# Performance work log

Hardware: AMD Instinct MI355X
Metric: run time of the kernel (lower is better)

## Reference

```python
import jax, jax.numpy as jnp
import numpy as np

LN_EPS = 1e-5

def _mlp(h, W1, b1, g1, beta1, W2, b2):
    # Linear -> LayerNorm -> SiLU -> Linear (make_mlp with 2 layers, output_activation=None)
    h = h @ W1 + b1
    mu = h.mean(-1, keepdims=True)
    var = h.var(-1, keepdims=True)  # biased var, matches torch LayerNorm
    h = (h - mu) * jax.lax.rsqrt(var + LN_EPS) * g1 + beta1
    h = jax.nn.silu(h)
    return h @ W2 + b2

def setup_inputs() -> dict:
    key = jax.random.key(0)
    ks = jax.random.split(key, 8)
    N, E, H = 50000, 800000, 128
    def init_w(k, fan_in, fan_out):
        lim = 1.0 / np.sqrt(fan_in)
        return jax.random.uniform(k, (fan_in, fan_out), jnp.float32, -lim, lim)
    return {
        "x": jax.random.normal(ks[0], (N, H), jnp.float32),
        "edge_index": jax.random.randint(ks[1], (2, E), 0, N),
        "e": jax.random.normal(ks[2], (E, H), jnp.float32),
        # node network: in 2H (cat of x and sum-aggregated messages)
        "Wn1": init_w(ks[3], 2 * H, H), "bn1": jnp.zeros((H,), jnp.float32),
        "gn1": jnp.ones((H,), jnp.float32), "betan1": jnp.zeros((H,), jnp.float32),
        "Wn2": init_w(ks[4], H, H), "bn2": jnp.zeros((H,), jnp.float32),
        # edge network: in 3H (cat of x_out[start], x_out[end], e)
        "We1": init_w(ks[5], 3 * H, H), "be1": jnp.zeros((H,), jnp.float32),
        "ge1": jnp.ones((H,), jnp.float32), "betae1": jnp.zeros((H,), jnp.float32),
        "We2": init_w(ks[6], H, H), "be2": jnp.zeros((H,), jnp.float32),
    }

def reference(x, edge_index, e, Wn1, bn1, gn1, betan1, Wn2, bn2, We1, be1, ge1, betae1, We2, be2):
    start, end = edge_index[0], edge_index[1]
    # aggregation == 'sum': scatter_add of edge features onto destination nodes
    msgs = jax.ops.segment_sum(e, end, num_segments=x.shape[0])  # [N, H]
    node_inputs = jnp.concatenate([x, msgs], axis=-1)  # [N, 2H]
    x_out = _mlp(node_inputs, Wn1, bn1, gn1, betan1, Wn2, bn2) + x  # residual
    edge_inputs = jnp.concatenate([x_out[start], x_out[end], e], axis=-1)  # [E, 3H]
    e_out = _mlp(edge_inputs, We1, be1, ge1, betae1, We2, be2) + e  # residual
    return (x_out, e_out)
```

## Files before the change

kernel.cpp:

```cpp
#include <hip/hip_runtime.h>

#define H 128
#define LN_EPS 1e-5f

typedef __attribute__((ext_vector_type(8))) short bf16x8;
typedef __attribute__((ext_vector_type(4))) float f32x4;

__device__ __forceinline__ ushort f2bf(float f) {
    unsigned u = __builtin_bit_cast(unsigned, f);
    u += 0x7fffu + ((u >> 16) & 1u);
    return (ushort)(u >> 16);
}

__device__ __forceinline__ float bf2f(ushort u) {
    return __builtin_bit_cast(float, (unsigned)u << 16);
}

__device__ __forceinline__ unsigned cvt_pk(float lo, float hi) {
    unsigned r;
    asm("v_cvt_pk_bf16_f32 %0, %1, %2" : "=v"(r) : "v"(lo), "v"(hi));
    return r;
}

__device__ __forceinline__ f32x4 mfma16(bf16x8 a, bf16x8 b, f32x4 c) {
    return __builtin_amdgcn_mfma_f32_16x16x32_bf16(a, b, c, 0, 0, 0);
}

__global__ __launch_bounds__(256) void hist_kernel(
    const int* __restrict__ ei, int* __restrict__ cnt, int E)
{
    int i = blockIdx.x * 256 + threadIdx.x;
    if (i < E) atomicAdd(&cnt[ei[E + i]], 1);
}

__global__ __launch_bounds__(1024) void scan_kernel(
    const int* __restrict__ cnt, int* __restrict__ off,
    int* __restrict__ cursor, int N)
{
    __shared__ int s[1024];
    const int t = threadIdx.x;
    const int chunk = (N + 1023) / 1024;
    const int lo = t * chunk, hi = min(lo + chunk, N);
    int sum = 0;
    for (int i = lo; i < hi; ++i) sum += cnt[i];
    s[t] = sum;
    __syncthreads();
    for (int d = 1; d < 1024; d <<= 1) {
        int v = (t >= d) ? s[t - d] : 0;
        __syncthreads();
        s[t] += v;
        __syncthreads();
    }
    int running = s[t] - sum;
    for (int i = lo; i < hi; ++i) {
        off[i] = running;
        cursor[i] = running;
        running += cnt[i];
    }
    if (t == 1023) off[N] = running;
}

__global__ __launch_bounds__(256) void reorder_kernel(
    const int* __restrict__ ei, int* __restrict__ cursor,
    int* __restrict__ sorted, int E)
{
    int i = blockIdx.x * 256 + threadIdx.x;
    if (i < E) {
        int pos = atomicAdd(&cursor[ei[E + i]], 1);
        sorted[pos] = i;
    }
}

__global__ __launch_bounds__(256) void segsum_kernel(
    const float* __restrict__ e, const int* __restrict__ sorted,
    const int* __restrict__ off, float* __restrict__ msgs, int N)
{
    int node = blockIdx.x * 4 + (threadIdx.x >> 6);
    int lane = threadIdx.x & 63;
    if (node >= N) return;
    int beg = off[node], end = off[node + 1];
    float ax = 0.f, ay = 0.f;
    for (int base = beg; base < end; base += 64) {
        int eid_l = (base + lane < end) ? sorted[base + lane] : 0;
        int cnt = min(64, end - base);
        int i = 0;
        for (; i + 4 <= cnt; i += 4) {
            int e0 = __shfl(eid_l, i), e1 = __shfl(eid_l, i + 1);
            int e2 = __shfl(eid_l, i + 2), e3 = __shfl(eid_l, i + 3);
            float2 v0 = *reinterpret_cast<const float2*>(e + (size_t)e0 * H + lane * 2);
            float2 v1 = *reinterpret_cast<const float2*>(e + (size_t)e1 * H + lane * 2);
            float2 v2 = *reinterpret_cast<const float2*>(e + (size_t)e2 * H + lane * 2);
            float2 v3 = *reinterpret_cast<const float2*>(e + (size_t)e3 * H + lane * 2);
            ax += v0.x + v1.x + v2.x + v3.x;
            ay += v0.y + v1.y + v2.y + v3.y;
        }
        for (; i < cnt; ++i) {
            int eid = __shfl(eid_l, i);
            float2 v = *reinterpret_cast<const float2*>(e + (size_t)eid * H + lane * 2);
            ax += v.x; ay += v.y;
        }
    }
    *reinterpret_cast<float2*>(msgs + (size_t)node * H + lane * 2) = make_float2(ax, ay);
}

__global__ __launch_bounds__(256) void wtrans_kernel(
    const float* __restrict__ W, ushort* __restrict__ Wt, int K)
{
    int idx = blockIdx.x * 256 + threadIdx.x;
    if (idx >= K * H) return;
    int k = idx >> 7, n = idx & (H - 1);
    Wt[n * K + k] = f2bf(W[idx]);
}

__global__ __launch_bounds__(256, 3) void node_mlp_kernel(
    const float* __restrict__ x, const float* __restrict__ msgs,
    const ushort* __restrict__ W1t, const float* __restrict__ b1,
    const float* __restrict__ g1, const float* __restrict__ be1,
    const ushort* __restrict__ W2t, const float* __restrict__ b2,
    const ushort* __restrict__ We1t,
    float* __restrict__ x_out,
    ushort* __restrict__ Pa, ushort* __restrict__ Pb, int N)
{
    __shared__ ushort smem[64 * 264];
    __shared__ float part_s[2][64], part_q[2][64];

    const int tid = threadIdx.x;
    const int row0 = blockIdx.x * 64;

    for (int idx = tid; idx < 64 * 64; idx += 256) {
        int r = idx >> 6, c4 = idx & 63;
        int row = row0 + r;
        float4 v = make_float4(0.f, 0.f, 0.f, 0.f);
        if (row < N)
            v = (c4 < 32) ? reinterpret_cast<const float4*>(x + (size_t)row * H)[c4]
                          : reinterpret_cast<const float4*>(msgs + (size_t)row * H)[c4 - 32];
        uint2 pk = make_uint2(cvt_pk(v.x, v.y), cvt_pk(v.z, v.w));
        *reinterpret_cast<uint2*>(&smem[r * 264 + c4 * 4]) = pk;
    }
    __syncthreads();

    const int lane = tid & 63, w = tid >> 6;
    const int l15 = lane & 15, lg = lane >> 4;
    const int mrow = (w & 1) * 32, ncol = (w >> 1) * 64;
    const int rA0 = mrow + l15, rA1 = mrow + 16 + l15;

    const ushort* pi0 = smem + (size_t)rA0 * 264;
    const ushort* pi1 = smem + (size_t)rA1 * 264;
    const ushort* pw1 = W1t + (size_t)(ncol + l15) * 256;

    f32x4 acc[2][4];
    #pragma unroll
    for (int mt = 0; mt < 2; ++mt)
        #pragma unroll
        for (int nt = 0; nt < 4; ++nt)
            acc[mt][nt] = (f32x4){0.f, 0.f, 0.f, 0.f};

    #pragma unroll
    for (int ks = 0; ks < 8; ++ks) {
        int k0 = ks * 32 + lg * 8;
        bf16x8 a0 = *reinterpret_cast<const bf16x8*>(pi0 + k0);
        bf16x8 a1 = *reinterpret_cast<const bf16x8*>(pi1 + k0);
        #pragma unroll
        for (int nt = 0; nt < 4; ++nt) {
            bf16x8 bfr = *reinterpret_cast<const bf16x8*>(pw1 + (size_t)nt * 16 * 256 + k0);
            acc[0][nt] = mfma16(a0, bfr, acc[0][nt]);
            acc[1][nt] = mfma16(a1, bfr, acc[1][nt]);
        }
    }

    float b1c[4], g1c[4], be1c[4];
    #pragma unroll
    for (int nt = 0; nt < 4; ++nt) {
        int c = ncol + nt * 16 + l15;
        b1c[nt] = b1[c]; g1c[nt] = g1[c]; be1c[nt] = be1[c];
    }
    #pragma unroll
    for (int mt = 0; mt < 2; ++mt)
        #pragma unroll
        for (int nt = 0; nt < 4; ++nt)
            #pragma unroll
            for (int r = 0; r < 4; ++r)
                acc[mt][nt][r] += b1c[nt];

    #pragma unroll
    for (int mt = 0; mt < 2; ++mt) {
        #pragma unroll
        for (int r = 0; r < 4; ++r) {
            float s = acc[mt][0][r] + acc[mt][1][r] + acc[mt][2][r] + acc[mt][3][r];
            float q = acc[mt][0][r] * acc[mt][0][r] + acc[mt][1][r] * acc[mt][1][r]
                    + acc[mt][2][r] * acc[mt][2][r] + acc[mt][3][r] * acc[mt][3][r];
            #pragma unroll
            for (int m = 8; m >= 1; m >>= 1) {
                s += __shfl_xor(s, m);
                q += __shfl_xor(q, m);
            }
            if (l15 == 0) {
                int rl = mrow + mt * 16 + lg * 4 + r;
                part_s[w >> 1][rl] = s;
                part_q[w >> 1][rl] = q;
            }
        }
    }
    __syncthreads();

    #pragma unroll
    for (int mt = 0; mt < 2; ++mt) {
        #pragma unroll
        for (int r = 0; r < 4; ++r) {
            int rl = mrow + mt * 16 + lg * 4 + r;
            float s  = part_s[0][rl] + part_s[1][rl];
            float q  = part_q[0][rl] + part_q[1][rl];
            float mu = s * (1.0f / H);
            float rs = rsqrtf(q * (1.0f / H) - mu * mu + LN_EPS);
            #pragma unroll
            for (int nt = 0; nt < 4; ++nt) {
                float v = (acc[mt][nt][r] - mu) * rs * g1c[nt] + be1c[nt];
                v = v / (1.0f + __expf(-v));
                smem[rl * 136 + ncol + nt * 16 + l15] = f2bf(v);
            }
        }
    }
    __syncthreads();

    const ushort* ph0 = smem + (size_t)rA0 * 136;
    const ushort* ph1 = smem + (size_t)rA1 * 136;
    const ushort* pw2 = W2t + (size_t)(ncol + l15) * 128;

    f32x4 acc2[2][4];
    #pragma unroll
    for (int nt = 0; nt < 4; ++nt) {
        float bb = b2[ncol + nt * 16 + l15];
        #pragma unroll
        for (int mt = 0; mt < 2; ++mt)
            acc2[mt][nt] = (f32x4){bb, bb, bb, bb};
    }
    #pragma unroll
    for (int ks = 0; ks < 4; ++ks) {
        int k0 = ks * 32 + lg * 8;
        bf16x8 a0 = *reinterpret_cast<const bf16x8*>(ph0 + k0);
        bf16x8 a1 = *reinterpret_cast<const bf16x8*>(ph1 + k0);
        #pragma unroll
        for (int nt = 0; nt < 4; ++nt) {
            bf16x8 bfr = *reinterpret_cast<const bf16x8*>(pw2 + (size_t)nt * 16 * 128 + k0);
            acc2[0][nt] = mfma16(a0, bfr, acc2[0][nt]);
            acc2[1][nt] = mfma16(a1, bfr, acc2[1][nt]);
        }
    }

    #pragma unroll
    for (int mt = 0; mt < 2; ++mt) {
        #pragma unroll
        for (int r = 0; r < 4; ++r) {
            int row = row0 + mrow + mt * 16 + lg * 4 + r;
            if (row < N) {
                const float* rp = x + (size_t)row * H;
                float* op = x_out + (size_t)row * H;
                #pragma unroll
                for (int nt = 0; nt < 4; ++nt) {
                    int c = ncol + nt * 16 + l15;
                    float o = acc2[mt][nt][r] + rp[c];
                    op[c] = o;
                    acc2[mt][nt][r] = o;
                }
            }
        }
    }
    __syncthreads();

    #pragma unroll
    for (int mt = 0; mt < 2; ++mt) {
        #pragma unroll
        for (int r = 0; r < 4; ++r) {
            int rl = mrow + mt * 16 + lg * 4 + r;
            #pragma unroll
            for (int nt = 0; nt < 4; ++nt)
                smem[rl * 136 + ncol + nt * 16 + l15] = f2bf(acc2[mt][nt][r]);
        }
    }
    __syncthreads();

    const ushort* px0 = smem + (size_t)rA0 * 136 + lg * 8;
    const ushort* px1 = smem + (size_t)rA1 * 136 + lg * 8;
    const ushort* pwa = We1t + (size_t)(ncol + l15) * 384 + lg * 8;
    const ushort* pwb = pwa + 128;

    f32x4 aa[2][4], ab[2][4];
    #pragma unroll
    for (int mt = 0; mt < 2; ++mt)
        #pragma unroll
        for (int nt = 0; nt < 4; ++nt) {
            aa[mt][nt] = (f32x4){0.f, 0.f, 0.f, 0.f};
            ab[mt][nt] = (f32x4){0.f, 0.f, 0.f, 0.f};
        }

    #pragma unroll
    for (int t = 0; t < 4; ++t) {
        bf16x8 a0 = *reinterpret_cast<const bf16x8*>(px0 + t * 32);
        bf16x8 a1 = *reinterpret_cast<const bf16x8*>(px1 + t * 32);
        #pragma unroll
        for (int nt = 0; nt < 4; ++nt) {
            bf16x8 ba = *reinterpret_cast<const bf16x8*>(pwa + (size_t)nt * 16 * 384 + t * 32);
            bf16x8 bb = *reinterpret_cast<const bf16x8*>(pwb + (size_t)nt * 16 * 384 + t * 32);
            aa[0][nt] = mfma16(a0, ba, aa[0][nt]);
            aa[1][nt] = mfma16(a1, ba, aa[1][nt]);
            ab[0][nt] = mfma16(a0, bb, ab[0][nt]);
            ab[1][nt] = mfma16(a1, bb, ab[1][nt]);
        }
    }

    #pragma unroll
    for (int mt = 0; mt < 2; ++mt) {
        #pragma unroll
        for (int r = 0; r < 4; ++r) {
            int row = row0 + mrow + mt * 16 + lg * 4 + r;
            if (row < N) {
                ushort* pa = Pa + (size_t)row * H;
                ushort* pb = Pb + (size_t)row * H;
                #pragma unroll
                for (int nt = 0; nt < 4; ++nt) {
                    int c = ncol + nt * 16 + l15;
                    pa[c] = f2bf(aa[mt][nt][r]);
                    pb[c] = f2bf(ab[mt][nt][r]);
                }
            }
        }
    }
}

__global__ __launch_bounds__(256, 4) void edge_mlp_kernel(
    const ushort* __restrict__ Pa, const ushort* __restrict__ Pb,
    const float* __restrict__ e, const int* __restrict__ ei,
    const ushort* __restrict__ W1t,
    const float* __restrict__ b1,
    const float* __restrict__ g1, const float* __restrict__ be1,
    const ushort* __restrict__ W2t, const float* __restrict__ b2,
    float* __restrict__ e_out, int E)
{
    __shared__ ushort es[64 * 136];
    __shared__ ushort ps[64 * 136];
    __shared__ float part_s[2][64], part_q[2][64];

    const int tid = threadIdx.x;
    const int row0 = blockIdx.x * 64;

    for (int idx = tid; idx < 64 * 16; idx += 256) {
        int r = idx >> 4, c = idx & 15;
        int rr = min(row0 + r, E - 1);
        int s = ei[rr], d = ei[E + rr];
        bf16x8 va = *reinterpret_cast<const bf16x8*>(Pa + (size_t)s * H + c * 8);
        bf16x8 vb = *reinterpret_cast<const bf16x8*>(Pb + (size_t)d * H + c * 8);
        float f0 = bf2f((ushort)va[0]) + bf2f((ushort)vb[0]);
        float f1 = bf2f((ushort)va[1]) + bf2f((ushort)vb[1]);
        float f2 = bf2f((ushort)va[2]) + bf2f((ushort)vb[2]);
        float f3 = bf2f((ushort)va[3]) + bf2f((ushort)vb[3]);
        float f4 = bf2f((ushort)va[4]) + bf2f((ushort)vb[4]);
        float f5 = bf2f((ushort)va[5]) + bf2f((ushort)vb[5]);
        float f6 = bf2f((ushort)va[6]) + bf2f((ushort)vb[6]);
        float f7 = bf2f((ushort)va[7]) + bf2f((ushort)vb[7]);
        uint4 pk = make_uint4(cvt_pk(f0, f1), cvt_pk(f2, f3),
                              cvt_pk(f4, f5), cvt_pk(f6, f7));
        *reinterpret_cast<uint4*>(&ps[r * 136 + c * 8]) = pk;
    }

    for (int idx = tid; idx < 64 * 32; idx += 256) {
        int r = idx >> 5, c4 = idx & 31;
        int row = row0 + r;
        float4 v = make_float4(0.f, 0.f, 0.f, 0.f);
        if (row < E)
            v = reinterpret_cast<const float4*>(e + (size_t)row * H)[c4];
        uint2 pk = make_uint2(cvt_pk(v.x, v.y), cvt_pk(v.z, v.w));
        *reinterpret_cast<uint2*>(&es[r * 136 + c4 * 4]) = pk;
    }
    __syncthreads();

    const int lane = tid & 63, w = tid >> 6;
    const int l15 = lane & 15, lg = lane >> 4;
    const int mrow = (w & 1) * 32, ncol = (w >> 1) * 64;
    const int rA0 = mrow + l15, rA1 = mrow + 16 + l15;

    const ushort* pe0 = es + (size_t)rA0 * 136 + lg * 8;
    const ushort* pe1 = es + (size_t)rA1 * 136 + lg * 8;
    const ushort* pw1 = W1t + (size_t)(ncol + l15) * 384 + 256 + lg * 8;

    f32x4 acc[2][4];
    #pragma unroll
    for (int mt = 0; mt < 2; ++mt)
        #pragma unroll
        for (int nt = 0; nt < 4; ++nt)
            acc[mt][nt] = (f32x4){0.f, 0.f, 0.f, 0.f};

    #pragma unroll
    for (int t = 0; t < 4; ++t) {
        bf16x8 a0 = *reinterpret_cast<const bf16x8*>(pe0 + t * 32);
        bf16x8 a1 = *reinterpret_cast<const bf16x8*>(pe1 + t * 32);
        #pragma unroll
        for (int nt = 0; nt < 4; ++nt) {
            bf16x8 bfr = *reinterpret_cast<const bf16x8*>(pw1 + (size_t)nt * 16 * 384 + t * 32);
            acc[0][nt] = mfma16(a0, bfr, acc[0][nt]);
            acc[1][nt] = mfma16(a1, bfr, acc[1][nt]);
        }
    }

    float b1c[4], g1c[4], be1c[4];
    #pragma unroll
    for (int nt = 0; nt < 4; ++nt) {
        int c = ncol + nt * 16 + l15;
        b1c[nt] = b1[c]; g1c[nt] = g1[c]; be1c[nt] = be1[c];
    }
    #pragma unroll
    for (int mt = 0; mt < 2; ++mt)
        #pragma unroll
        for (int r = 0; r < 4; ++r) {
            int rl = mrow + mt * 16 + lg * 4 + r;
            #pragma unroll
            for (int nt = 0; nt < 4; ++nt)
                acc[mt][nt][r] += b1c[nt] + bf2f(ps[rl * 136 + ncol + nt * 16 + l15]);
        }

    #pragma unroll
    for (int mt = 0; mt < 2; ++mt) {
        #pragma unroll
        for (int r = 0; r < 4; ++r) {
            float s = acc[mt][0][r] + acc[mt][1][r] + acc[mt][2][r] + acc[mt][3][r];
            float q = acc[mt][0][r] * acc[mt][0][r] + acc[mt][1][r] * acc[mt][1][r]
                    + acc[mt][2][r] * acc[mt][2][r] + acc[mt][3][r] * acc[mt][3][r];
            #pragma unroll
            for (int m = 8; m >= 1; m >>= 1) {
                s += __shfl_xor(s, m);
                q += __shfl_xor(q, m);
            }
            if (l15 == 0) {
                int rl = mrow + mt * 16 + lg * 4 + r;
                part_s[w >> 1][rl] = s;
                part_q[w >> 1][rl] = q;
            }
        }
    }
    __syncthreads();

    #pragma unroll
    for (int mt = 0; mt < 2; ++mt) {
        #pragma unroll
        for (int r = 0; r < 4; ++r) {
            int rl = mrow + mt * 16 + lg * 4 + r;
            float s  = part_s[0][rl] + part_s[1][rl];
            float q  = part_q[0][rl] + part_q[1][rl];
            float mu = s * (1.0f / H);
            float rs = rsqrtf(q * (1.0f / H) - mu * mu + LN_EPS);
            #pragma unroll
            for (int nt = 0; nt < 4; ++nt) {
                float v = (acc[mt][nt][r] - mu) * rs * g1c[nt] + be1c[nt];
                v = v / (1.0f + __expf(-v));
                es[rl * 136 + ncol + nt * 16 + l15] = f2bf(v);
            }
        }
    }
    __syncthreads();

    const ushort* ph0 = es + (size_t)rA0 * 136;
    const ushort* ph1 = es + (size_t)rA1 * 136;
    const ushort* pw2 = W2t + (size_t)(ncol + l15) * 128;

    f32x4 acc2[2][4];
    #pragma unroll
    for (int nt = 0; nt < 4; ++nt) {
        float bb = b2[ncol + nt * 16 + l15];
        #pragma unroll
        for (int mt = 0; mt < 2; ++mt)
            acc2[mt][nt] = (f32x4){bb, bb, bb, bb};
    }
    #pragma unroll
    for (int ks = 0; ks < 4; ++ks) {
        int k0 = ks * 32 + lg * 8;
        bf16x8 a0 = *reinterpret_cast<const bf16x8*>(ph0 + k0);
        bf16x8 a1 = *reinterpret_cast<const bf16x8*>(ph1 + k0);
        #pragma unroll
        for (int nt = 0; nt < 4; ++nt) {
            bf16x8 bfr = *reinterpret_cast<const bf16x8*>(pw2 + (size_t)nt * 16 * 128 + k0);
            acc2[0][nt] = mfma16(a0, bfr, acc2[0][nt]);
            acc2[1][nt] = mfma16(a1, bfr, acc2[1][nt]);
        }
    }

    #pragma unroll
    for (int mt = 0; mt < 2; ++mt) {
        #pragma unroll
        for (int r = 0; r < 4; ++r) {
            int row = row0 + mrow + mt * 16 + lg * 4 + r;
            if (row < E) {
                const float* rp = e + (size_t)row * H;
                float* op = e_out + (size_t)row * H;
                #pragma unroll
                for (int nt = 0; nt < 4; ++nt) {
                    int c = ncol + nt * 16 + l15;
                    op[c] = acc2[mt][nt][r] + rp[c];
                }
            }
        }
    }
}

extern "C" void kernel_launch(void* const* d_in, const int* in_sizes, int n_in,
                              void* d_out, int out_size, void* d_ws, size_t ws_size,
                              hipStream_t stream)
{
    const float* x     = (const float*)d_in[0];
    const int*   ei    = (const int*)  d_in[1];
    const float* e     = (const float*)d_in[2];
    const float* Wn1   = (const float*)d_in[3];
    const float* bn1   = (const float*)d_in[4];
    const float* gn1   = (const float*)d_in[5];
    const float* betan1= (const float*)d_in[6];
    const float* Wn2   = (const float*)d_in[7];
    const float* bn2   = (const float*)d_in[8];
    const float* We1   = (const float*)d_in[9];
    const float* be1   = (const float*)d_in[10];
    const float* ge1   = (const float*)d_in[11];
    const float* betae1= (const float*)d_in[12];
    const float* We2   = (const float*)d_in[13];
    const float* be2   = (const float*)d_in[14];

    const int N = in_sizes[0] / H;
    const int E = in_sizes[2] / H;

    float* x_out = (float*)d_out;
    float* e_out = (float*)d_out + (long long)N * H;

    char* p = (char*)d_ws;
    float*  msgs = (float*)p;            p += (size_t)N * H * sizeof(float);
    ushort* Pa   = (ushort*)p;           p += (size_t)N * H * sizeof(ushort);
    ushort* Pb   = (ushort*)p;           p += (size_t)N * H * sizeof(ushort);
    ushort* Wn1t = (ushort*)p;           p += (size_t)256 * H * sizeof(ushort);
    ushort* Wn2t = (ushort*)p;           p += (size_t)H * H * sizeof(ushort);
    ushort* We1t = (ushort*)p;           p += (size_t)384 * H * sizeof(ushort);
    ushort* We2t = (ushort*)p;           p += (size_t)H * H * sizeof(ushort);
    p = (char*)(((size_t)p + 15) & ~(size_t)15);
    int* cnt    = (int*)p;               p += (size_t)N * sizeof(int);
    int* off    = (int*)p;               p += ((size_t)N + 1) * sizeof(int);
    int* cursor = (int*)p;               p += (size_t)N * sizeof(int);
    int* sorted = (int*)p;               p += (size_t)E * sizeof(int);

    wtrans_kernel<<<(256 * H + 255) / 256, 256, 0, stream>>>(Wn1, Wn1t, 256);
    wtrans_kernel<<<(H * H + 255) / 256, 256, 0, stream>>>(Wn2, Wn2t, H);
    wtrans_kernel<<<(384 * H + 255) / 256, 256, 0, stream>>>(We1, We1t, 384);
    wtrans_kernel<<<(H * H + 255) / 256, 256, 0, stream>>>(We2, We2t, H);

    hipMemsetAsync(cnt, 0, (size_t)N * sizeof(int), stream);
    hist_kernel<<<(E + 255) / 256, 256, 0, stream>>>(ei, cnt, E);
    scan_kernel<<<1, 1024, 0, stream>>>(cnt, off, cursor, N);
    reorder_kernel<<<(E + 255) / 256, 256, 0, stream>>>(ei, cursor, sorted, E);
    segsum_kernel<<<(N + 3) / 4, 256, 0, stream>>>(e, sorted, off, msgs, N);

    {
        int blocks = (N + 63) / 64;
        node_mlp_kernel<<<blocks, 256, 0, stream>>>(
            x, msgs, Wn1t, bn1, gn1, betan1, Wn2t, bn2, We1t,
            x_out, Pa, Pb, N);
    }
    {
        int blocks = (E + 63) / 64;
        edge_mlp_kernel<<<blocks, 256, 0, stream>>>(
            Pa, Pb, e, ei, We1t, be1, ge1, betae1, We2t, be2, e_out, E);
    }
}
```

Measured before the change: 761.4 us.

## Stash a bf16 copy of edge features during segsum for reuse in edge MLP

The segment-sum kernel, which already reads every fp32 edge feature row, now also writes a bf16 copy into workspace. The edge MLP kernel then loads that half-width copy for both its tile input and its residual add, instead of re-reading the fp32 edges. This is meant to cut the edge kernel's read traffic, at the price of an extra full-size write pass in segsum. The residual is now added from bf16 values, which lowers output precision. The new path only runs when the workspace is large enough, with a fallback template otherwise.

```diff
diff --git a/kernel.cpp b/kernel.cpp
--- a/kernel.cpp
+++ b/kernel.cpp
@@ -73,7 +73,8 @@
 
 __global__ __launch_bounds__(256) void segsum_kernel(
     const float* __restrict__ e, const int* __restrict__ sorted,
-    const int* __restrict__ off, float* __restrict__ msgs, int N)
+    const int* __restrict__ off, float* __restrict__ msgs,
+    ushort* __restrict__ ebf, int N)
 {
     int node = blockIdx.x * 4 + (threadIdx.x >> 6);
     int lane = threadIdx.x & 63;
@@ -91,12 +92,20 @@
             float2 v1 = *reinterpret_cast<const float2*>(e + (size_t)e1 * H + lane * 2);
             float2 v2 = *reinterpret_cast<const float2*>(e + (size_t)e2 * H + lane * 2);
             float2 v3 = *reinterpret_cast<const float2*>(e + (size_t)e3 * H + lane * 2);
+            if (ebf) {
+                *reinterpret_cast<unsigned*>(ebf + (size_t)e0 * H + lane * 2) = cvt_pk(v0.x, v0.y);
+                *reinterpret_cast<unsigned*>(ebf + (size_t)e1 * H + lane * 2) = cvt_pk(v1.x, v1.y);
+                *reinterpret_cast<unsigned*>(ebf + (size_t)e2 * H + lane * 2) = cvt_pk(v2.x, v2.y);
+                *reinterpret_cast<unsigned*>(ebf + (size_t)e3 * H + lane * 2) = cvt_pk(v3.x, v3.y);
+            }
             ax += v0.x + v1.x + v2.x + v3.x;
             ay += v0.y + v1.y + v2.y + v3.y;
         }
         for (; i < cnt; ++i) {
             int eid = __shfl(eid_l, i);
             float2 v = *reinterpret_cast<const float2*>(e + (size_t)eid * H + lane * 2);
+            if (ebf)
+                *reinterpret_cast<unsigned*>(ebf + (size_t)eid * H + lane * 2) = cvt_pk(v.x, v.y);
             ax += v.x; ay += v.y;
         }
     }
@@ -327,9 +336,11 @@
     }
 }
 
+template<bool EBF>
 __global__ __launch_bounds__(256, 4) void edge_mlp_kernel(
     const ushort* __restrict__ Pa, const ushort* __restrict__ Pb,
-    const float* __restrict__ e, const int* __restrict__ ei,
+    const float* __restrict__ e, const ushort* __restrict__ ebf,
+    const int* __restrict__ ei,
     const ushort* __restrict__ W1t,
     const float* __restrict__ b1,
     const float* __restrict__ g1, const float* __restrict__ be1,
@@ -362,14 +373,25 @@
         *reinterpret_cast<uint4*>(&ps[r * 136 + c * 8]) = pk;
     }
 
-    for (int idx = tid; idx < 64 * 32; idx += 256) {
-        int r = idx >> 5, c4 = idx & 31;
-        int row = row0 + r;
-        float4 v = make_float4(0.f, 0.f, 0.f, 0.f);
-        if (row < E)
-            v = reinterpret_cast<const float4*>(e + (size_t)row * H)[c4];
-        uint2 pk = make_uint2(cvt_pk(v.x, v.y), cvt_pk(v.z, v.w));
-        *reinterpret_cast<uint2*>(&es[r * 136 + c4 * 4]) = pk;
+    if constexpr (EBF) {
+        for (int idx = tid; idx < 64 * 16; idx += 256) {
+            int r = idx >> 4, c = idx & 15;
+            int row = row0 + r;
+            bf16x8 v = (bf16x8){0,0,0,0,0,0,0,0};
+            if (row < E)
+                v = *reinterpret_cast<const bf16x8*>(ebf + (size_t)row * H + c * 8);
+            *reinterpret_cast<bf16x8*>(&es[r * 136 + c * 8]) = v;
+        }
+    } else {
+        for (int idx = tid; idx < 64 * 32; idx += 256) {
+            int r = idx >> 5, c4 = idx & 31;
+            int row = row0 + r;
+            float4 v = make_float4(0.f, 0.f, 0.f, 0.f);
+            if (row < E)
+                v = reinterpret_cast<const float4*>(e + (size_t)row * H)[c4];
+            uint2 pk = make_uint2(cvt_pk(v.x, v.y), cvt_pk(v.z, v.w));
+            *reinterpret_cast<uint2*>(&es[r * 136 + c4 * 4]) = pk;
+        }
     }
     __syncthreads();
 
@@ -488,12 +510,14 @@
         for (int r = 0; r < 4; ++r) {
             int row = row0 + mrow + mt * 16 + lg * 4 + r;
             if (row < E) {
-                const float* rp = e + (size_t)row * H;
                 float* op = e_out + (size_t)row * H;
                 #pragma unroll
                 for (int nt = 0; nt < 4; ++nt) {
                     int c = ncol + nt * 16 + l15;
-                    op[c] = acc2[mt][nt][r] + rp[c];
+                    float res;
+                    if constexpr (EBF) res = bf2f(ebf[(size_t)row * H + c]);
+                    else               res = e[(size_t)row * H + c];
+                    op[c] = acc2[mt][nt][r] + res;
                 }
             }
         }
@@ -526,7 +550,8 @@
     float* x_out = (float*)d_out;
     float* e_out = (float*)d_out + (long long)N * H;
 
-    char* p = (char*)d_ws;
+    char* p0 = (char*)d_ws;
+    char* p = p0;
     float*  msgs = (float*)p;            p += (size_t)N * H * sizeof(float);
     ushort* Pa   = (ushort*)p;           p += (size_t)N * H * sizeof(ushort);
     ushort* Pb   = (ushort*)p;           p += (size_t)N * H * sizeof(ushort);
@@ -539,6 +564,10 @@
     int* off    = (int*)p;               p += ((size_t)N + 1) * sizeof(int);
     int* cursor = (int*)p;               p += (size_t)N * sizeof(int);
     int* sorted = (int*)p;               p += (size_t)E * sizeof(int);
+    p = (char*)(((size_t)p + 15) & ~(size_t)15);
+    ushort* ebf = (ushort*)p;            p += (size_t)E * H * sizeof(ushort);
+
+    const bool use_ebf = ((size_t)(p - p0) <= ws_size);
 
     wtrans_kernel<<<(256 * H + 255) / 256, 256, 0, stream>>>(Wn1, Wn1t, 256);
     wtrans_kernel<<<(H * H + 255) / 256, 256, 0, stream>>>(Wn2, Wn2t, H);
@@ -549,7 +578,8 @@
     hist_kernel<<<(E + 255) / 256, 256, 0, stream>>>(ei, cnt, E);
     scan_kernel<<<1, 1024, 0, stream>>>(cnt, off, cursor, N);
     reorder_kernel<<<(E + 255) / 256, 256, 0, stream>>>(ei, cursor, sorted, E);
-    segsum_kernel<<<(N + 3) / 4, 256, 0, stream>>>(e, sorted, off, msgs, N);
+    segsum_kernel<<<(N + 3) / 4, 256, 0, stream>>>(
+        e, sorted, off, msgs, use_ebf ? ebf : nullptr, N);
 
     {
         int blocks = (N + 63) / 64;
@@ -559,7 +589,11 @@
     }
     {
         int blocks = (E + 63) / 64;
-        edge_mlp_kernel<<<blocks, 256, 0, stream>>>(
-            Pa, Pb, e, ei, We1t, be1, ge1, betae1, We2t, be2, e_out, E);
-    }
-}
+        if (use_ebf)
+            edge_mlp_kernel<true><<<blocks, 256, 0, stream>>>(
+                Pa, Pb, e, ebf, ei, We1t, be1, ge1, betae1, We2t, be2, e_out, E);
+        else
+            edge_mlp_kernel<false><<<blocks, 256, 0, stream>>>(
+                Pa, Pb, e, ebf, ei, We1t, be1, ge1, betae1, We2t, be2, e_out, E);
+    }
+}
```

Result: slower. 838.2 us (+10.1%).
